# Optimization experiments

Measured on AMD Instinct MI355X. Metric: run time of the kernel, lower is better.

Reference implementation:

```python
import jax, jax.numpy as jnp
import numpy as np

N_LAYERS = 4
GAMMA = 0.5
D_MODEL = 256
D_STATE = 64
D_CONV = 4
EXPAND = 2
D_INNER = EXPAND * D_MODEL            # 512 (= headdim, so nheads = 1)
NHEADS = 1
CONV_DIM = D_INNER + 2 * D_STATE      # 640
D_IN_PROJ = 2 * D_INNER + 2 * D_STATE + NHEADS  # 1153
VOCAB = 100
VOCAB_PAD = 104                        # padded to multiple of 8 by MambaConfig
BATCH = 8
SEQ = 2048


def setup_inputs() -> dict:
    key = jax.random.key(0)
    ks = jax.random.split(key, 8)
    def nrm(k, shape):
        # gamma init: std = 1 / d1**gamma, d1 = shape[0]
        return (jax.random.normal(k, shape, jnp.float32) * (1.0 / shape[0] ** GAMMA))
    inp = {}
    inp["input_ids"] = jax.random.randint(ks[0], (BATCH, SEQ), 0, VOCAB)
    inp["embed"] = nrm(ks[1], (VOCAB_PAD, D_MODEL))          # tied embedding / lm_head
    inp["in_proj_w"] = nrm(ks[2], (N_LAYERS * D_IN_PROJ, D_MODEL)).reshape(N_LAYERS, D_IN_PROJ, D_MODEL)
    inp["conv_w"] = nrm(ks[3], (N_LAYERS * CONV_DIM, D_CONV)).reshape(N_LAYERS, CONV_DIM, D_CONV)
    inp["conv_b"] = jnp.zeros((N_LAYERS, CONV_DIM), jnp.float32)
    inp["dt_bias"] = jax.random.uniform(ks[4], (N_LAYERS, NHEADS), jnp.float32, -4.0, -1.0)
    inp["A_log"] = jnp.log(jax.random.uniform(ks[5], (N_LAYERS, NHEADS), jnp.float32, 1.0, 16.0))
    inp["Dparam"] = jnp.ones((N_LAYERS, NHEADS), jnp.float32)
    inp["norm_g_w"] = jnp.ones((N_LAYERS, D_INNER), jnp.float32)
    inp["out_proj_w"] = nrm(ks[6], (N_LAYERS * D_MODEL, D_INNER)).reshape(N_LAYERS, D_MODEL, D_INNER)
    inp["block_norm_w"] = jnp.ones((N_LAYERS, D_MODEL), jnp.float32)
    inp["norm_f_w"] = jnp.ones((D_MODEL,), jnp.float32)
    return inp


def rmsnorm(x, w, eps=1e-5):
    return x * jax.lax.rsqrt(jnp.mean(x * x, axis=-1, keepdims=True) + eps) * w


def ssm_scan(x, dt, A, Bc, Cc):
    # x: (B,L,P)  dt: (B,L)  A: scalar  Bc,Cc: (B,L,N). Sequential selective scan.
    def step(h, inp):  # h: (B,P,N)
        x_t, dt_t, b_t, c_t = inp
        h = h * jnp.exp(dt_t * A)[:, None, None] + (dt_t[:, None] * x_t)[:, :, None] * b_t[:, None, :]
        y = jnp.einsum('bpn,bn->bp', h, c_t)
        return h, y
    h0 = jnp.zeros((x.shape[0], x.shape[2], Bc.shape[2]), x.dtype)
    xs = (jnp.swapaxes(x, 0, 1), jnp.swapaxes(dt, 0, 1), jnp.swapaxes(Bc, 0, 1), jnp.swapaxes(Cc, 0, 1))
    _, ys = jax.lax.scan(step, h0, xs)
    return jnp.swapaxes(ys, 0, 1)  # (B,L,P)


def mamba2_mixer(h, ipw, cw, cb, dtb, alog, dp, ngw, opw):
    zxbcdt = h @ ipw.T                                   # (B,L,1153)
    z = zxbcdt[..., :D_INNER]
    xBC = zxbcdt[..., D_INNER:D_INNER + CONV_DIM]
    dt_raw = zxbcdt[..., D_INNER + CONV_DIM:]            # (B,L,1)
    # depthwise causal conv1d (kernel D_CONV) + SiLU
    xp = jnp.pad(xBC, ((0, 0), (D_CONV - 1, 0), (0, 0)))
    L = xBC.shape[1]
    conv = sum(xp[:, k:k + L, :] * cw[:, k] for k in range(D_CONV)) + cb
    xBC = jax.nn.silu(conv)
    x = xBC[..., :D_INNER]
    Bc = xBC[..., D_INNER:D_INNER + D_STATE]
    Cc = xBC[..., D_INNER + D_STATE:]
    dt = jax.nn.softplus(dt_raw[..., 0] + dtb[0])        # (B,L), nheads=1
    A = -jnp.exp(alog[0])
    y = ssm_scan(x, dt, A, Bc, Cc) + dp[0] * x
    y = rmsnorm(y * jax.nn.silu(z), ngw)                 # RMSNormGated (norm after gate)
    return y @ opw.T


def reference(input_ids, embed, in_proj_w, conv_w, conv_b, dt_bias, A_log, Dparam,
              norm_g_w, out_proj_w, block_norm_w, norm_f_w):
    hidden = embed[input_ids]                            # (B,L,D_MODEL)
    residual = None
    for i in range(N_LAYERS):
        residual = hidden if residual is None else hidden + residual
        hidden = rmsnorm(residual, block_norm_w[i])
        hidden = mamba2_mixer(hidden, in_proj_w[i], conv_w[i], conv_b[i], dt_bias[i],
                              A_log[i], Dparam[i], norm_g_w[i], out_proj_w[i])
    residual = hidden + residual
    final = rmsnorm(residual, norm_f_w)
    logits = final @ embed.T                             # tied lm_head, (B,L,VOCAB_PAD)
    return logits[:, -1, :VOCAB]                         # last-token logits, (B,VOCAB)
```

## Files before the change

kernel.cpp:

```cpp
#include <hip/hip_runtime.h>
#include <math.h>

#define NB    8
#define LSEQ  2048
#define TKN   16384
#define DM    256
#define DI    512
#define DS    64
#define DIP   1153
#define DIPP  1160
#define CDIM  640
#define NL    4
#define NC    16
#define CL    128
#define VOC   100

typedef short bf16x8 __attribute__((ext_vector_type(8)));
typedef short bf16x4 __attribute__((ext_vector_type(4)));
typedef float f32x4  __attribute__((ext_vector_type(4)));
typedef unsigned short ushort_t;

__device__ __forceinline__ unsigned short f2bf(float f) {
  unsigned int u = __float_as_uint(f);
  unsigned int r = u + 0x7FFFu + ((u >> 16) & 1u);
  return (unsigned short)(r >> 16);
}
__device__ __forceinline__ float bf2f(unsigned short u) {
  return __uint_as_float(((unsigned int)u) << 16);
}

__global__ __launch_bounds__(256) void prologue(const float* __restrict__ ipw,
    const float* __restrict__ opw, ushort_t* __restrict__ wbi, ushort_t* __restrict__ wbo,
    const int* __restrict__ ids, const float* __restrict__ embed,
    float* __restrict__ resid, ushort_t* __restrict__ hn, const float* __restrict__ w0) {
  int blk = blockIdx.x;
  if (blk < TKN / 4) {
    int wave = threadIdx.x >> 6, lane = threadIdx.x & 63;
    int t = blk * 4 + wave;
    size_t o = (size_t)t * DM + lane * 4;
    int id = ids[t];
    float4 r4 = *(const float4*)&embed[(size_t)id * DM + lane * 4];
    *(float4*)&resid[o] = r4;
    float ss = r4.x * r4.x + r4.y * r4.y + r4.z * r4.z + r4.w * r4.w;
    #pragma unroll
    for (int m = 32; m >= 1; m >>= 1) ss += __shfl_xor(ss, m, 64);
    float sc = rsqrtf(ss * (1.f / DM) + 1e-5f);
    float4 w4 = *(const float4*)&w0[lane * 4];
    bf16x4 o4;
    o4[0] = (short)f2bf(r4.x * sc * w4.x);
    o4[1] = (short)f2bf(r4.y * sc * w4.y);
    o4[2] = (short)f2bf(r4.z * sc * w4.z);
    o4[3] = (short)f2bf(r4.w * sc * w4.w);
    *(bf16x4*)&hn[o] = o4;
  } else {
    const int n1 = NL * DIP * DM;
    const int n2 = NL * DM * DI;
    int i4 = ((blk - TKN / 4) * 256 + threadIdx.x) * 4;
    if (i4 < n1) {
      float4 v = *(const float4*)(ipw + i4);
      bf16x4 o; o[0] = (short)f2bf(v.x); o[1] = (short)f2bf(v.y);
      o[2] = (short)f2bf(v.z); o[3] = (short)f2bf(v.w);
      *(bf16x4*)(wbi + i4) = o;
    } else {
      int j = i4 - n1;
      if (j < n2) {
        float4 v = *(const float4*)(opw + j);
        bf16x4 o; o[0] = (short)f2bf(v.x); o[1] = (short)f2bf(v.y);
        o[2] = (short)f2bf(v.z); o[3] = (short)f2bf(v.w);
        *(bf16x4*)(wbo + j) = o;
      }
    }
  }
}

#define LSTR  40
#define LSTR2 72
__global__ __launch_bounds__(256) void gemm_nt_bf16(const ushort_t* __restrict__ A,
    const ushort_t* __restrict__ Bw, ushort_t* __restrict__ C, int N, int K, int ldc) {
  __shared__ short sA[128 * LSTR2];
  __shared__ short sB[128 * LSTR2];
  int tid = threadIdx.x;
  int bn = blockIdx.x * 128;
  int bm = blockIdx.y * 128;
  int wave = tid >> 6, lane = tid & 63;
  int wm = (wave >> 1) * 64, wn = (wave & 1) * 64;
  int q = lane >> 4, c = lane & 15;

  f32x4 acc[4][4];
  #pragma unroll
  for (int i = 0; i < 4; ++i)
    #pragma unroll
    for (int j = 0; j < 4; ++j) acc[i][j] = (f32x4)0.f;

  int sr = tid >> 1;
  int sc = (tid & 1) * 32;
  const ushort_t* Ag = A + (size_t)(bm + sr) * K + sc;
  const ushort_t* Bg = Bw + (size_t)(bn + sr) * K + sc;
  bool bok = (bn + sr) < N;
  short* sAp = &sA[sr * LSTR2 + sc];
  short* sBp = &sB[sr * LSTR2 + sc];

  for (int k0 = 0; k0 < K; k0 += 64) {
    bf16x8 a0 = *(const bf16x8*)(Ag + k0);
    bf16x8 a1 = *(const bf16x8*)(Ag + k0 + 8);
    bf16x8 a2 = *(const bf16x8*)(Ag + k0 + 16);
    bf16x8 a3 = *(const bf16x8*)(Ag + k0 + 24);
    bf16x8 b0 = (bf16x8)(short)0, b1 = (bf16x8)(short)0;
    bf16x8 b2 = (bf16x8)(short)0, b3 = (bf16x8)(short)0;
    if (bok) {
      b0 = *(const bf16x8*)(Bg + k0);
      b1 = *(const bf16x8*)(Bg + k0 + 8);
      b2 = *(const bf16x8*)(Bg + k0 + 16);
      b3 = *(const bf16x8*)(Bg + k0 + 24);
    }
    __syncthreads();
    *(bf16x8*)(sAp)      = a0;
    *(bf16x8*)(sAp + 8)  = a1;
    *(bf16x8*)(sAp + 16) = a2;
    *(bf16x8*)(sAp + 24) = a3;
    *(bf16x8*)(sBp)      = b0;
    *(bf16x8*)(sBp + 8)  = b1;
    *(bf16x8*)(sBp + 16) = b2;
    *(bf16x8*)(sBp + 24) = b3;
    __syncthreads();
    #pragma unroll
    for (int ks = 0; ks < 2; ++ks) {
      bf16x8 af[4], bfr[4];
      #pragma unroll
      for (int i = 0; i < 4; ++i)
        af[i] = *(const bf16x8*)&sA[(wm + i * 16 + c) * LSTR2 + ks * 32 + q * 8];
      #pragma unroll
      for (int j = 0; j < 4; ++j)
        bfr[j] = *(const bf16x8*)&sB[(wn + j * 16 + c) * LSTR2 + ks * 32 + q * 8];
      #pragma unroll
      for (int i = 0; i < 4; ++i)
        #pragma unroll
        for (int j = 0; j < 4; ++j)
          acc[i][j] = __builtin_amdgcn_mfma_f32_16x16x32_bf16(af[i], bfr[j], acc[i][j], 0, 0, 0);
    }
  }
  #pragma unroll
  for (int i = 0; i < 4; ++i) {
    int m = bm + wm + i * 16 + q * 4;
    #pragma unroll
    for (int j = 0; j < 4; ++j) {
      int n = bn + wn + j * 16 + c;
      if (n < N) {
        #pragma unroll
        for (int r = 0; r < 4; ++r)
          C[(size_t)(m + r) * ldc + n] = f2bf(acc[i][j][r]);
      }
    }
  }
}

__global__ __launch_bounds__(256) void outproj_norm(const ushort_t* __restrict__ yb,
    const ushort_t* __restrict__ zx, const ushort_t* __restrict__ Bw,
    const float* __restrict__ gw, float* __restrict__ resid,
    const float* __restrict__ wnext, ushort_t* __restrict__ hn) {
  __shared__ short sA[32 * LSTR];
  __shared__ short sB[256 * LSTR];
  __shared__ float swl[DI];
  __shared__ float swn[DM];
  __shared__ float rs[128];
  __shared__ float rs2[32 * 2];
  int tid = threadIdx.x;
  int bm = blockIdx.x * 32;
  int wave = tid >> 6, lane = tid & 63;
  int wm = (wave >> 1) * 16, wn = (wave & 1) * 128;
  int q = lane >> 4, c = lane & 15;
  swl[tid] = gw[tid];
  swl[tid + 256] = gw[tid + 256];
  swn[tid] = wnext[tid];

  f32x4 acc[8];
  #pragma unroll
  for (int j = 0; j < 8; ++j) acc[j] = (f32x4)0.f;

  int ar = tid >> 2, ak = (tid & 3) * 8;
  bool isa = tid < 128;
  const ushort_t* yrow = yb + (size_t)(bm + ar) * DI + ak;
  const ushort_t* zrow = zx + (size_t)(bm + ar) * DIPP + ak;
  const ushort_t* Bg = Bw + (size_t)tid * DI;
  float sumsq = 0.f;
  __syncthreads();

  for (int k0 = 0; k0 < DI; k0 += 32) {
    bf16x8 g8;
    if (isa) {
      bf16x8 y8 = *(const bf16x8*)(yrow + k0);
      bf16x8 z8 = *(const bf16x8*)(zrow + k0);
      #pragma unroll
      for (int e = 0; e < 8; ++e) {
        float zz = bf2f((ushort_t)z8[e]);
        float gg = bf2f((ushort_t)y8[e]) * (zz / (1.f + __expf(-zz)));
        sumsq += gg * gg;
        g8[e] = (short)f2bf(gg * swl[k0 + ak + e]);
      }
    }
    bf16x8 b0 = *(const bf16x8*)(Bg + k0);
    bf16x8 b1 = *(const bf16x8*)(Bg + k0 + 8);
    bf16x8 b2 = *(const bf16x8*)(Bg + k0 + 16);
    bf16x8 b3 = *(const bf16x8*)(Bg + k0 + 24);
    __syncthreads();
    if (isa) *(bf16x8*)&sA[ar * LSTR + ak] = g8;
    *(bf16x8*)&sB[tid * LSTR]      = b0;
    *(bf16x8*)&sB[tid * LSTR + 8]  = b1;
    *(bf16x8*)&sB[tid * LSTR + 16] = b2;
    *(bf16x8*)&sB[tid * LSTR + 24] = b3;
    __syncthreads();
    bf16x8 af = *(const bf16x8*)&sA[(wm + c) * LSTR + q * 8];
    #pragma unroll
    for (int j = 0; j < 8; ++j) {
      bf16x8 bfr = *(const bf16x8*)&sB[(wn + j * 16 + c) * LSTR + q * 8];
      acc[j] = __builtin_amdgcn_mfma_f32_16x16x32_bf16(af, bfr, acc[j], 0, 0, 0);
    }
  }
  if (isa) rs[tid] = sumsq;
  __syncthreads();

  float outv[8][4];
  float sq2[4];
  #pragma unroll
  for (int r = 0; r < 4; ++r) {
    int row = wm + q * 4 + r;
    float s1 = rsqrtf((rs[row * 4] + rs[row * 4 + 1] + rs[row * 4 + 2] + rs[row * 4 + 3])
                      * (1.f / DI) + 1e-5f);
    float sq = 0.f;
    #pragma unroll
    for (int j = 0; j < 8; ++j) {
      int col = wn + j * 16 + c;
      size_t ro = (size_t)(bm + row) * DM + col;
      float rn = resid[ro] + s1 * acc[j][r];
      resid[ro] = rn;
      outv[j][r] = rn;
      sq += rn * rn;
    }
    sq2[r] = sq;
  }
  #pragma unroll
  for (int r = 0; r < 4; ++r) {
    #pragma unroll
    for (int m = 1; m <= 8; m <<= 1) sq2[r] += __shfl_xor(sq2[r], m, 64);
  }
  if (c == 0) {
    #pragma unroll
    for (int r = 0; r < 4; ++r)
      rs2[(wm + q * 4 + r) * 2 + (wave & 1)] = sq2[r];
  }
  __syncthreads();
  #pragma unroll
  for (int r = 0; r < 4; ++r) {
    int row = wm + q * 4 + r;
    float s2 = rsqrtf((rs2[row * 2] + rs2[row * 2 + 1]) * (1.f / DM) + 1e-5f);
    #pragma unroll
    for (int j = 0; j < 8; ++j) {
      int col = wn + j * 16 + c;
      hn[(size_t)(bm + row) * DM + col] = f2bf(outv[j][r] * s2 * swn[col]);
    }
  }
}

__global__ __launch_bounds__(256) void conv_silu(const ushort_t* __restrict__ zx,
    const float* __restrict__ cw, const float* __restrict__ cb,
    const float* __restrict__ dtbias, ushort_t* __restrict__ xo,
    ushort_t* __restrict__ Bo, ushort_t* __restrict__ Co, ushort_t* __restrict__ Ut,
    float* __restrict__ dtb, float* __restrict__ csumb) {
  __shared__ ushort_t tile[67 * 128];
  __shared__ ushort_t tt[128 * 72];
  int tid = threadIdx.x;
  int ct = blockIdx.x, tb_ = blockIdx.y, b = blockIdx.z;
  size_t rowb = (size_t)b * LSEQ;
  if (ct == 5) {
    if (tb_ < 16 && tid < 64) {
      int lane = tid;
      size_t base = rowb + (size_t)tb_ * CL;
      float bias = dtbias[0];
      float x0 = bf2f(zx[(base + 2 * lane) * DIPP + (DIP - 1)]) + bias;
      float x1 = bf2f(zx[(base + 2 * lane + 1) * DIPP + (DIP - 1)]) + bias;
      float d0 = (x0 > 20.f) ? x0 : log1pf(__expf(x0));
      float d1 = (x1 > 20.f) ? x1 : log1pf(__expf(x1));
      dtb[base + 2 * lane] = d0;
      dtb[base + 2 * lane + 1] = d1;
      float p = d0 + d1;
      #pragma unroll
      for (int off = 1; off < 64; off <<= 1) {
        float t = __shfl_up(p, off, 64);
        if (lane >= off) p += t;
      }
      csumb[base + 2 * lane]     = p - d1;
      csumb[base + 2 * lane + 1] = p;
    }
    return;
  }
  int c0 = ct * 128, l0 = tb_ * 64;
  bool isx = (ct < 4);
  for (int slot = tid; slot < 67 * 16; slot += 256) {
    int r = slot >> 4, gg = slot & 15;
    int l = l0 + r - 3;
    bf16x8 v = (bf16x8)(short)0;
    if (l >= 0) v = *(const bf16x8*)&zx[(rowb + l) * DIPP + DI + c0 + gg * 8];
    *(bf16x8*)&tile[r * 128 + gg * 8] = v;
  }
  int g = tid & 15, tq = tid >> 4;
  int cbase = c0 + g * 8;
  float w[4][8], bias[8];
  #pragma unroll
  for (int e = 0; e < 8; ++e) {
    float4 wv = *(const float4*)&cw[(cbase + e) * 4];
    w[0][e] = wv.x; w[1][e] = wv.y; w[2][e] = wv.z; w[3][e] = wv.w;
    bias[e] = cb[cbase + e];
  }
  __syncthreads();
  bf16x8 rows[7];
  #pragma unroll
  for (int r = 0; r < 7; ++r)
    rows[r] = *(const bf16x8*)&tile[(tq * 4 + r) * 128 + g * 8];
  #pragma unroll
  for (int it = 0; it < 4; ++it) {
    int t = tq * 4 + it;
    size_t tl = rowb + l0 + t;
    bf16x8 o;
    #pragma unroll
    for (int e = 0; e < 8; ++e) {
      float s = bias[e]
              + w[0][e] * bf2f((ushort_t)rows[it][e])
              + w[1][e] * bf2f((ushort_t)rows[it + 1][e])
              + w[2][e] * bf2f((ushort_t)rows[it + 2][e])
              + w[3][e] * bf2f((ushort_t)rows[it + 3][e]);
      float v = s / (1.f + __expf(-s));
      o[e] = (short)f2bf(v);
      if (isx) tt[(g * 8 + e) * 72 + t] = (ushort_t)o[e];
    }
    if (isx) {
      *(bf16x8*)&xo[tl * DI + cbase] = o;
    } else if (g < 8) {
      *(bf16x8*)&Bo[tl * DS + (cbase - DI)] = o;
    } else {
      *(bf16x8*)&Co[tl * DS + (cbase - DI - DS)] = o;
    }
  }
  if (isx) {
    __syncthreads();
    #pragma unroll
    for (int pass = 0; pass < 4; ++pass) {
      int slot = pass * 256 + tid;
      int op = slot >> 3, sg = slot & 7;
      bf16x8 v = *(const bf16x8*)&tt[op * 72 + sg * 8];
      *(bf16x8*)&Ut[((size_t)b * DI + c0 + op) * LSEQ + l0 + sg * 8] = v;
    }
  }
}

__global__ __launch_bounds__(256) void state_gemm(const ushort_t* __restrict__ Bb,
    const ushort_t* __restrict__ Ut, const float* __restrict__ csumb,
    const float* __restrict__ dtb, const float* __restrict__ alog,
    float* __restrict__ hst) {
  __shared__ short sW[64 * 144];
  __shared__ short sX[128 * 40];
  __shared__ float scs[128];
  __shared__ float sdt[128];
  int tid = threadIdx.x;
  int ph = blockIdx.x, ch = blockIdx.y, b = blockIdx.z;
  int bc = b * NC + ch;
  size_t tb = (size_t)b * LSEQ + ch * CL;
  float Aval = -expf(alog[0]);
  if (tid < 128) { scs[tid] = csumb[tb + tid]; sdt[tid] = dtb[tb + tid]; }
  __syncthreads();
  float Stot = scs[127];
  {
    int s = tid >> 1, noff = (tid & 1) * 32;
    float scale = __expf(Aval * (Stot - scs[s])) * sdt[s];
    #pragma unroll
    for (int blk = 0; blk < 4; ++blk) {
      bf16x8 v = *(const bf16x8*)&Bb[(tb + s) * DS + noff + blk * 8];
      #pragma unroll
      for (int e = 0; e < 8; ++e)
        sW[(noff + blk * 8 + e) * 144 + s] = (short)f2bf(bf2f((ushort_t)v[e]) * scale);
    }
  }
  int wave = tid >> 6, lane = tid & 63;
  int wn = (wave >> 1) * 32, wp = (wave & 1) * 64;
  int q = lane >> 4, c = lane & 15;
  f32x4 acc[2][4];
  #pragma unroll
  for (int i = 0; i < 2; ++i)
    #pragma unroll
    for (int j = 0; j < 4; ++j) acc[i][j] = (f32x4)0.f;

  for (int ks = 0; ks < 4; ++ks) {
    __syncthreads();
    {
      int r = tid >> 1, off = (tid & 1) * 16;
      size_t ua = ((size_t)b * DI + ph * 128 + r) * LSEQ + ch * CL + ks * 32 + off;
      bf16x8 u0 = *(const bf16x8*)&Ut[ua];
      bf16x8 u1 = *(const bf16x8*)&Ut[ua + 8];
      *(bf16x8*)&sX[r * 40 + off]     = u0;
      *(bf16x8*)&sX[r * 40 + off + 8] = u1;
    }
    __syncthreads();
    bf16x8 af[2], bfr[4];
    #pragma unroll
    for (int i = 0; i < 2; ++i)
      af[i] = *(const bf16x8*)&sW[(wn + i * 16 + c) * 144 + ks * 32 + q * 8];
    #pragma unroll
    for (int j = 0; j < 4; ++j)
      bfr[j] = *(const bf16x8*)&sX[(wp + j * 16 + c) * 40 + q * 8];
    #pragma unroll
    for (int i = 0; i < 2; ++i)
      #pragma unroll
      for (int j = 0; j < 4; ++j)
        acc[i][j] = __builtin_amdgcn_mfma_f32_16x16x32_bf16(af[i], bfr[j], acc[i][j], 0, 0, 0);
  }
  #pragma unroll
  for (int i = 0; i < 2; ++i) {
    int n = wn + i * 16 + q * 4;
    #pragma unroll
    for (int j = 0; j < 4; ++j) {
      int pg = ph * 128 + wp + j * 16 + c;
      #pragma unroll
      for (int r = 0; r < 4; ++r)
        hst[((size_t)bc * DS + n + r) * DI + pg] = acc[i][j][r];
    }
  }
}

__global__ __launch_bounds__(256) void combine2(const float* __restrict__ hst,
    const float* __restrict__ csumb, const float* __restrict__ alog,
    ushort_t* __restrict__ hin) {
  __shared__ ushort_t ts[64 * 17];
  int tid = threadIdx.x;
  int pt = blockIdx.x, nt = blockIdx.y, b = blockIdx.z;
  int p0 = pt * 64, n0 = nt * 16;
  int pl = tid & 63, ng = tid >> 6;
  float Aval = -expf(alog[0]);
  float h[4];
  #pragma unroll
  for (int i = 0; i < 4; ++i) h[i] = 0.f;
  for (int c = 0; c < NC; ++c) {
    int bc = b * NC + c;
    #pragma unroll
    for (int i = 0; i < 4; ++i)
      ts[pl * 17 + ng * 4 + i] = f2bf(h[i]);
    __syncthreads();
    {
      int on = tid & 15;
      #pragma unroll
      for (int pass = 0; pass < 4; ++pass) {
        int op = (tid >> 4) + pass * 16;
        hin[((size_t)bc * DI + p0 + op) * DS + n0 + on] = ts[op * 17 + on];
      }
    }
    __syncthreads();
    float Sc = csumb[(size_t)b * LSEQ + c * CL + CL - 1];
    float dec = __expf(Aval * Sc);
    #pragma unroll
    for (int i = 0; i < 4; ++i) {
      float loc = hst[((size_t)bc * DS + n0 + ng * 4 + i) * DI + p0 + pl];
      h[i] = h[i] * dec + loc;
    }
  }
}

__global__ __launch_bounds__(256) void y_gemm(const ushort_t* __restrict__ Bb,
    const ushort_t* __restrict__ Cb, const ushort_t* __restrict__ Ut,
    const ushort_t* __restrict__ hin, const float* __restrict__ csumb,
    const float* __restrict__ dtb, const float* __restrict__ alog,
    const float* __restrict__ dpar, const ushort_t* __restrict__ xb,
    ushort_t* __restrict__ y) {
  __shared__ short sC[128 * 72];
  __shared__ short sM[128 * 136];
  __shared__ short sU[128 * 80];
  __shared__ float scs[128];
  __shared__ float sdt[128];
  int tid = threadIdx.x;
  int ph = blockIdx.x, ch = blockIdx.y, b = blockIdx.z;
  int bc = b * NC + ch;
  size_t tb = (size_t)b * LSEQ + ch * CL;
  float Aval = -expf(alog[0]);
  float dp = dpar[0];
  int wave = tid >> 6, lane = tid & 63;
  int q = lane >> 4, c = lane & 15;

  {
    int r = tid >> 1, off = (tid & 1) * 32;
    #pragma unroll
    for (int blk = 0; blk < 4; ++blk) {
      *(bf16x8*)&sC[r * 72 + off + blk * 8] = *(const bf16x8*)&Cb[(tb + r) * DS + off + blk * 8];
      *(bf16x8*)&sU[r * 80 + off + blk * 8] = *(const bf16x8*)&Bb[(tb + r) * DS + off + blk * 8];
    }
  }
  if (tid < 128) { scs[tid] = csumb[tb + tid]; sdt[tid] = dtb[tb + tid]; }
  __syncthreads();

  {
    int wm = (wave >> 1) * 64, wss = (wave & 1) * 64;
    if (wave == 1) {
      #pragma unroll
      for (int i = 0; i < 4; ++i) {
        #pragma unroll
        for (int r = 0; r < 4; ++r) {
          int t = i * 16 + q * 4 + r;
          #pragma unroll
          for (int j = 0; j < 4; ++j)
            sM[t * 136 + 64 + j * 16 + c] = 0;
        }
      }
    } else {
      f32x4 g[4][4];
      #pragma unroll
      for (int i = 0; i < 4; ++i)
        #pragma unroll
        for (int j = 0; j < 4; ++j) g[i][j] = (f32x4)0.f;
      #pragma unroll
      for (int k0 = 0; k0 < 64; k0 += 32) {
        bf16x8 af[4], bfr[4];
        #pragma unroll
        for (int i = 0; i < 4; ++i)
          af[i] = *(const bf16x8*)&sC[(wm + i * 16 + c) * 72 + k0 + q * 8];
        #pragma unroll
        for (int j = 0; j < 4; ++j)
          bfr[j] = *(const bf16x8*)&sU[(wss + j * 16 + c) * 80 + k0 + q * 8];
        #pragma unroll
        for (int i = 0; i < 4; ++i)
          #pragma unroll
          for (int j = 0; j < 4; ++j)
            g[i][j] = __builtin_amdgcn_mfma_f32_16x16x32_bf16(af[i], bfr[j], g[i][j], 0, 0, 0);
      }
      float dts[4];
      #pragma unroll
      for (int j = 0; j < 4; ++j) dts[j] = sdt[wss + j * 16 + c];
      #pragma unroll
      for (int i = 0; i < 4; ++i) {
        #pragma unroll
        for (int r = 0; r < 4; ++r) {
          int t = wm + i * 16 + q * 4 + r;
          float ct = scs[t];
          #pragma unroll
          for (int j = 0; j < 4; ++j) {
            int s = wss + j * 16 + c;
            float v = g[i][j][r];
            float m = (s <= t) ? v * __expf(Aval * (ct - scs[s])) * dts[j] : 0.f;
            sM[t * 136 + s] = (short)f2bf(m);
          }
        }
      }
    }
  }

  int wm2 = (wave >> 1) * 64, wp = (wave & 1) * 64;
  f32x4 acc[4][4];
  #pragma unroll
  for (int i = 0; i < 4; ++i)
    #pragma unroll
    for (int j = 0; j < 4; ++j) acc[i][j] = (f32x4)0.f;

  for (int ks = 0; ks < 4; ++ks) {
    __syncthreads();
    {
      int r = tid >> 1, off = (tid & 1) * 16;
      size_t ua = ((size_t)b * DI + ph * 128 + r) * LSEQ + ch * CL + ks * 32 + off;
      bf16x8 u0 = *(const bf16x8*)&Ut[ua];
      bf16x8 u1 = *(const bf16x8*)&Ut[ua + 8];
      *(bf16x8*)&sU[r * 40 + off]     = u0;
      *(bf16x8*)&sU[r * 40 + off + 8] = u1;
    }
    __syncthreads();
    if (!(wm2 == 0 && ks >= 2)) {
      bf16x8 af[4], bfr[4];
      #pragma unroll
      for (int i = 0; i < 4; ++i)
        af[i] = *(const bf16x8*)&sM[(wm2 + i * 16 + c) * 136 + ks * 32 + q * 8];
      #pragma unroll
      for (int j = 0; j < 4; ++j)
        bfr[j] = *(const bf16x8*)&sU[(wp + j * 16 + c) * 40 + q * 8];
      #pragma unroll
      for (int i = 0; i < 4; ++i)
        #pragma unroll
        for (int j = 0; j < 4; ++j)
          acc[i][j] = __builtin_amdgcn_mfma_f32_16x16x32_bf16(af[i], bfr[j], acc[i][j], 0, 0, 0);
    }
  }

  __syncthreads();
  {
    int r = tid >> 1, off = (tid & 1) * 32;
    float sc_t = __expf(Aval * scs[r]);
    #pragma unroll
    for (int blk = 0; blk < 4; ++blk) {
      bf16x8 v = *(const bf16x8*)&sC[r * 72 + off + blk * 8];
      bf16x8 o;
      #pragma unroll
      for (int e = 0; e < 8; ++e)
        o[e] = (short)f2bf(bf2f((ushort_t)v[e]) * sc_t);
      *(bf16x8*)&sM[r * 80 + off + blk * 8] = o;
    }
  }
  for (int ks = 4; ks < 6; ++ks) {
    __syncthreads();
    {
      int r = tid >> 1, off = (tid & 1) * 16;
      size_t ha = ((size_t)bc * DI + ph * 128 + r) * DS + (ks - 4) * 32 + off;
      bf16x8 h0 = *(const bf16x8*)&hin[ha];
      bf16x8 h1 = *(const bf16x8*)&hin[ha + 8];
      *(bf16x8*)&sU[r * 40 + off]     = h0;
      *(bf16x8*)&sU[r * 40 + off + 8] = h1;
    }
    __syncthreads();
    bf16x8 af[4], bfr[4];
    #pragma unroll
    for (int i = 0; i < 4; ++i)
      af[i] = *(const bf16x8*)&sM[(wm2 + i * 16 + c) * 80 + (ks - 4) * 32 + q * 8];
    #pragma unroll
    for (int j = 0; j < 4; ++j)
      bfr[j] = *(const bf16x8*)&sU[(wp + j * 16 + c) * 40 + q * 8];
    #pragma unroll
    for (int i = 0; i < 4; ++i)
      #pragma unroll
      for (int j = 0; j < 4; ++j)
        acc[i][j] = __builtin_amdgcn_mfma_f32_16x16x32_bf16(af[i], bfr[j], acc[i][j], 0, 0, 0);
  }

  #pragma unroll
  for (int i = 0; i < 4; ++i) {
    #pragma unroll
    for (int r = 0; r < 4; ++r) {
      int t = wm2 + i * 16 + q * 4 + r;
      size_t row = (tb + t) * DI;
      #pragma unroll
      for (int j = 0; j < 4; ++j) {
        int pg = ph * 128 + wp + j * 16 + c;
        y[row + pg] = f2bf(acc[i][j][r] + dp * bf2f(xb[row + pg]));
      }
    }
  }
}

__global__ __launch_bounds__(256) void finalize(const ushort_t* __restrict__ hn,
    const float* __restrict__ embed, float* __restrict__ out) {
  int b = blockIdx.x, tid = threadIdx.x;
  __shared__ float fin[DM];
  size_t off = ((size_t)b * LSEQ + (LSEQ - 1)) * DM;
  fin[tid] = bf2f(hn[off + tid]);
  __syncthreads();
  if (tid < VOC) {
    float acc = 0.f;
    #pragma unroll 8
    for (int d = 0; d < DM; ++d) acc += fin[d] * embed[(size_t)tid * DM + d];
    out[b * VOC + tid] = acc;
  }
}

extern "C" void kernel_launch(void* const* d_in, const int* in_sizes, int n_in,
                              void* d_out, int out_size, void* d_ws, size_t ws_size,
                              hipStream_t stream) {
  const int*   ids   = (const int*)d_in[0];
  const float* embed = (const float*)d_in[1];
  const float* ipw   = (const float*)d_in[2];
  const float* cw    = (const float*)d_in[3];
  const float* cb    = (const float*)d_in[4];
  const float* dtbias= (const float*)d_in[5];
  const float* alog  = (const float*)d_in[6];
  const float* dpar  = (const float*)d_in[7];
  const float* ngw   = (const float*)d_in[8];
  const float* opw   = (const float*)d_in[9];
  const float* bnw   = (const float*)d_in[10];
  const float* nfw   = (const float*)d_in[11];
  float* out = (float*)d_out;

  char* p = (char*)d_ws;
  float* resid = (float*)p;            p += (size_t)TKN * DM * 4;
  ushort_t* hn = (ushort_t*)p;         p += (size_t)TKN * DM * 2;
  ushort_t* zx = (ushort_t*)p;         p += (size_t)TKN * DIPP * 2;
  float* dtb   = (float*)p;            p += (size_t)TKN * 4;
  float* csumb = (float*)p;            p += (size_t)TKN * 4;
  ushort_t* xb = (ushort_t*)p;         p += (size_t)TKN * DI * 2;
  ushort_t* yb = (ushort_t*)p;         p += (size_t)TKN * DI * 2;
  ushort_t* Bb = (ushort_t*)p;         p += (size_t)TKN * DS * 2;
  ushort_t* Cb = (ushort_t*)p;         p += (size_t)TKN * DS * 2;
  ushort_t* Ut = (ushort_t*)p;         p += (size_t)TKN * DI * 2;
  ushort_t* hin= (ushort_t*)p;         p += (size_t)NB * NC * DI * DS * 2;
  ushort_t* wbi= (ushort_t*)p;         p += (size_t)NL * DIP * DM * 2;
  ushort_t* wbo= (ushort_t*)p;         p += (size_t)NL * DM * DI * 2;
  float* hst = (float*)yb;

  const int convblks = (NL * DIP * DM + NL * DM * DI + 1023) / 1024;
  prologue<<<TKN / 4 + convblks, 256, 0, stream>>>(ipw, opw, wbi, wbo,
                                                   ids, embed, resid, hn, bnw);

  for (int i = 0; i < NL; ++i) {
    gemm_nt_bf16<<<dim3((DIP + 127) / 128, TKN / 128), 256, 0, stream>>>(
        hn, wbi + (size_t)i * DIP * DM, zx, DIP, DM, DIPP);
    conv_silu<<<dim3(6, LSEQ / 64, NB), 256, 0, stream>>>(
        zx, cw + (size_t)i * CDIM * 4, cb + (size_t)i * CDIM, dtbias + i,
        xb, Bb, Cb, Ut, dtb, csumb);
    state_gemm<<<dim3(4, NC, NB), 256, 0, stream>>>(Bb, Ut, csumb, dtb, alog + i, hst);
    combine2<<<dim3(DI / 64, 4, NB), 256, 0, stream>>>(hst, csumb, alog + i, hin);
    y_gemm<<<dim3(4, NC, NB), 256, 0, stream>>>(Bb, Cb, Ut, hin, csumb, dtb,
                                                alog + i, dpar + i, xb, yb);
    const float* wnext = (i < NL - 1) ? (bnw + (size_t)(i + 1) * DM) : nfw;
    outproj_norm<<<TKN / 32, 256, 0, stream>>>(
        yb, zx, wbo + (size_t)i * DM * DI, ngw + (size_t)i * DI, resid, wnext, hn);
  }

  finalize<<<NB, 256, 0, stream>>>(hn, embed, out);
}
```

Baseline: 544.0 us.

## Precompute masked C·Bᵀ decay matrix once per chunk in state_gemm, reuse in y_gemm

The intra-chunk masked decay matrix M (C·Bᵀ with exp decay and dt scaling) used to be rebuilt by every one of the 4 head-slice blocks in y_gemm. It is now computed once per (batch, chunk) by an extra block slice (ph==4) in state_gemm and written to a global bf16 buffer, which y_gemm then loads. y_gemm also scales C fragments in registers straight from global memory instead of staging them through shared memory, which cuts its LDS footprint. The cost is an extra global round trip of M (about 4MB per layer) and one more dependent block slice in state_gemm. The ph==4 blocks return early, with wave 1 doing no work and never writing the upper-right zero block. That block is never read, because y_gemm skips ks>=2 for rows 0-63.

```diff
diff --git a/kernel.cpp b/kernel.cpp
--- a/kernel.cpp
+++ b/kernel.cpp
@@ -353,11 +353,11 @@
 }
 
 __global__ __launch_bounds__(256) void state_gemm(const ushort_t* __restrict__ Bb,
-    const ushort_t* __restrict__ Ut, const float* __restrict__ csumb,
-    const float* __restrict__ dtb, const float* __restrict__ alog,
-    float* __restrict__ hst) {
-  __shared__ short sW[64 * 144];
-  __shared__ short sX[128 * 40];
+    const ushort_t* __restrict__ Cb, const ushort_t* __restrict__ Ut,
+    const float* __restrict__ csumb, const float* __restrict__ dtb,
+    const float* __restrict__ alog, float* __restrict__ hst,
+    ushort_t* __restrict__ Mbuf) {
+  __shared__ short smem[128 * 72 + 128 * 80];
   __shared__ float scs[128];
   __shared__ float sdt[128];
   int tid = threadIdx.x;
@@ -365,7 +365,71 @@
   int bc = b * NC + ch;
   size_t tb = (size_t)b * LSEQ + ch * CL;
   float Aval = -expf(alog[0]);
+  int wave = tid >> 6, lane = tid & 63;
+  int q = lane >> 4, c = lane & 15;
   if (tid < 128) { scs[tid] = csumb[tb + tid]; sdt[tid] = dtb[tb + tid]; }
+
+  if (ph == 4) {
+    short* sC = smem;
+    short* sB = smem + 128 * 72;
+    {
+      int r = tid >> 1, off = (tid & 1) * 32;
+      #pragma unroll
+      for (int blk = 0; blk < 4; ++blk) {
+        *(bf16x8*)&sC[r * 72 + off + blk * 8] = *(const bf16x8*)&Cb[(tb + r) * DS + off + blk * 8];
+        *(bf16x8*)&sB[r * 80 + off + blk * 8] = *(const bf16x8*)&Bb[(tb + r) * DS + off + blk * 8];
+      }
+    }
+    __syncthreads();
+    int wm = (wave >> 1) * 64, wss = (wave & 1) * 64;
+    if (wave == 1) return;
+    f32x4 g[4][4];
+    #pragma unroll
+    for (int i = 0; i < 4; ++i)
+      #pragma unroll
+      for (int j = 0; j < 4; ++j) g[i][j] = (f32x4)0.f;
+    #pragma unroll
+    for (int k0 = 0; k0 < 64; k0 += 32) {
+      bf16x8 af[4], bfr[4];
+      #pragma unroll
+      for (int i = 0; i < 4; ++i)
+        af[i] = *(const bf16x8*)&sC[(wm + i * 16 + c) * 72 + k0 + q * 8];
+      #pragma unroll
+      for (int j = 0; j < 4; ++j)
+        bfr[j] = *(const bf16x8*)&sB[(wss + j * 16 + c) * 80 + k0 + q * 8];
+      #pragma unroll
+      for (int i = 0; i < 4; ++i)
+        #pragma unroll
+        for (int j = 0; j < 4; ++j)
+          g[i][j] = __builtin_amdgcn_mfma_f32_16x16x32_bf16(af[i], bfr[j], g[i][j], 0, 0, 0);
+    }
+    float dts[4];
+    #pragma unroll
+    for (int j = 0; j < 4; ++j) dts[j] = sdt[wss + j * 16 + c];
+    ushort_t* Mrow = Mbuf + (size_t)bc * CL * CL;
+    #pragma unroll
+    for (int i = 0; i < 4; ++i) {
+      #pragma unroll
+      for (int r = 0; r < 4; ++r) {
+        int t = wm + i * 16 + q * 4 + r;
+        float ct = scs[t];
+        #pragma unroll
+        for (int j = 0; j < 4; ++j) {
+          int s = wss + j * 16 + c;
+          float v = g[i][j][r];
+          float m = (s <= t) ? v * __expf(Aval * (ct - scs[s])) * dts[j] : 0.f;
+          unsigned int mb = (unsigned int)f2bf(m);
+          unsigned int partner = __shfl_xor(mb, 1, 64);
+          if ((c & 1) == 0)
+            *(unsigned int*)&Mrow[t * CL + s] = mb | (partner << 16);
+        }
+      }
+    }
+    return;
+  }
+
+  short* sW = smem;
+  short* sX = smem + 64 * 144;
   __syncthreads();
   float Stot = scs[127];
   {
@@ -379,9 +443,7 @@
         sW[(noff + blk * 8 + e) * 144 + s] = (short)f2bf(bf2f((ushort_t)v[e]) * scale);
     }
   }
-  int wave = tid >> 6, lane = tid & 63;
   int wn = (wave >> 1) * 32, wp = (wave & 1) * 64;
-  int q = lane >> 4, c = lane & 15;
   f32x4 acc[2][4];
   #pragma unroll
   for (int i = 0; i < 2; ++i)
@@ -462,17 +524,14 @@
   }
 }
 
-__global__ __launch_bounds__(256) void y_gemm(const ushort_t* __restrict__ Bb,
+__global__ __launch_bounds__(256) void y_gemm(const ushort_t* __restrict__ Mbuf,
     const ushort_t* __restrict__ Cb, const ushort_t* __restrict__ Ut,
     const ushort_t* __restrict__ hin, const float* __restrict__ csumb,
-    const float* __restrict__ dtb, const float* __restrict__ alog,
-    const float* __restrict__ dpar, const ushort_t* __restrict__ xb,
-    ushort_t* __restrict__ y) {
-  __shared__ short sC[128 * 72];
+    const float* __restrict__ alog, const float* __restrict__ dpar,
+    const ushort_t* __restrict__ xb, ushort_t* __restrict__ y) {
   __shared__ short sM[128 * 136];
-  __shared__ short sU[128 * 80];
+  __shared__ short sU[128 * 40];
   __shared__ float scs[128];
-  __shared__ float sdt[128];
   int tid = threadIdx.x;
   int ph = blockIdx.x, ch = blockIdx.y, b = blockIdx.z;
   int bc = b * NC + ch;
@@ -483,72 +542,19 @@
   int q = lane >> 4, c = lane & 15;
 
   {
-    int r = tid >> 1, off = (tid & 1) * 32;
-    #pragma unroll
-    for (int blk = 0; blk < 4; ++blk) {
-      *(bf16x8*)&sC[r * 72 + off + blk * 8] = *(const bf16x8*)&Cb[(tb + r) * DS + off + blk * 8];
-      *(bf16x8*)&sU[r * 80 + off + blk * 8] = *(const bf16x8*)&Bb[(tb + r) * DS + off + blk * 8];
-    }
-  }
-  if (tid < 128) { scs[tid] = csumb[tb + tid]; sdt[tid] = dtb[tb + tid]; }
-  __syncthreads();
-
-  {
-    int wm = (wave >> 1) * 64, wss = (wave & 1) * 64;
-    if (wave == 1) {
-      #pragma unroll
-      for (int i = 0; i < 4; ++i) {
-        #pragma unroll
-        for (int r = 0; r < 4; ++r) {
-          int t = i * 16 + q * 4 + r;
-          #pragma unroll
-          for (int j = 0; j < 4; ++j)
-            sM[t * 136 + 64 + j * 16 + c] = 0;
-        }
-      }
-    } else {
-      f32x4 g[4][4];
-      #pragma unroll
-      for (int i = 0; i < 4; ++i)
-        #pragma unroll
-        for (int j = 0; j < 4; ++j) g[i][j] = (f32x4)0.f;
-      #pragma unroll
-      for (int k0 = 0; k0 < 64; k0 += 32) {
-        bf16x8 af[4], bfr[4];
-        #pragma unroll
-        for (int i = 0; i < 4; ++i)
-          af[i] = *(const bf16x8*)&sC[(wm + i * 16 + c) * 72 + k0 + q * 8];
-        #pragma unroll
-        for (int j = 0; j < 4; ++j)
-          bfr[j] = *(const bf16x8*)&sU[(wss + j * 16 + c) * 80 + k0 + q * 8];
-        #pragma unroll
-        for (int i = 0; i < 4; ++i)
-          #pragma unroll
-          for (int j = 0; j < 4; ++j)
-            g[i][j] = __builtin_amdgcn_mfma_f32_16x16x32_bf16(af[i], bfr[j], g[i][j], 0, 0, 0);
-      }
-      float dts[4];
-      #pragma unroll
-      for (int j = 0; j < 4; ++j) dts[j] = sdt[wss + j * 16 + c];
-      #pragma unroll
-      for (int i = 0; i < 4; ++i) {
-        #pragma unroll
-        for (int r = 0; r < 4; ++r) {
-          int t = wm + i * 16 + q * 4 + r;
-          float ct = scs[t];
-          #pragma unroll
-          for (int j = 0; j < 4; ++j) {
-            int s = wss + j * 16 + c;
-            float v = g[i][j][r];
-            float m = (s <= t) ? v * __expf(Aval * (ct - scs[s])) * dts[j] : 0.f;
-            sM[t * 136 + s] = (short)f2bf(m);
-          }
-        }
-      }
-    }
-  }
+    const ushort_t* Mrow = Mbuf + (size_t)bc * CL * CL;
+    #pragma unroll
+    for (int pass = 0; pass < 8; ++pass) {
+      int slot = pass * 256 + tid;
+      int t = slot >> 4, sg = slot & 15;
+      bf16x8 v = *(const bf16x8*)&Mrow[t * CL + sg * 8];
+      *(bf16x8*)&sM[t * 136 + sg * 8] = v;
+    }
+  }
+  if (tid < 128) scs[tid] = csumb[tb + tid];
 
   int wm2 = (wave >> 1) * 64, wp = (wave & 1) * 64;
+  int r2 = tid >> 1, off16 = (tid & 1) * 16;
   f32x4 acc[4][4];
   #pragma unroll
   for (int i = 0; i < 4; ++i)
@@ -558,12 +564,11 @@
   for (int ks = 0; ks < 4; ++ks) {
     __syncthreads();
     {
-      int r = tid >> 1, off = (tid & 1) * 16;
-      size_t ua = ((size_t)b * DI + ph * 128 + r) * LSEQ + ch * CL + ks * 32 + off;
+      size_t ua = ((size_t)b * DI + ph * 128 + r2) * LSEQ + ch * CL + ks * 32 + off16;
       bf16x8 u0 = *(const bf16x8*)&Ut[ua];
       bf16x8 u1 = *(const bf16x8*)&Ut[ua + 8];
-      *(bf16x8*)&sU[r * 40 + off]     = u0;
-      *(bf16x8*)&sU[r * 40 + off + 8] = u1;
+      *(bf16x8*)&sU[r2 * 40 + off16]     = u0;
+      *(bf16x8*)&sU[r2 * 40 + off16 + 8] = u1;
     }
     __syncthreads();
     if (!(wm2 == 0 && ks >= 2)) {
@@ -582,38 +587,31 @@
     }
   }
 
-  __syncthreads();
-  {
-    int r = tid >> 1, off = (tid & 1) * 32;
-    float sc_t = __expf(Aval * scs[r]);
-    #pragma unroll
-    for (int blk = 0; blk < 4; ++blk) {
-      bf16x8 v = *(const bf16x8*)&sC[r * 72 + off + blk * 8];
-      bf16x8 o;
-      #pragma unroll
-      for (int e = 0; e < 8; ++e)
-        o[e] = (short)f2bf(bf2f((ushort_t)v[e]) * sc_t);
-      *(bf16x8*)&sM[r * 80 + off + blk * 8] = o;
-    }
-  }
-  for (int ks = 4; ks < 6; ++ks) {
+  float rscale[4];
+  #pragma unroll
+  for (int i = 0; i < 4; ++i)
+    rscale[i] = __expf(Aval * scs[wm2 + i * 16 + c]);
+  for (int ks2 = 0; ks2 < 2; ++ks2) {
     __syncthreads();
     {
-      int r = tid >> 1, off = (tid & 1) * 16;
-      size_t ha = ((size_t)bc * DI + ph * 128 + r) * DS + (ks - 4) * 32 + off;
+      size_t ha = ((size_t)bc * DI + ph * 128 + r2) * DS + ks2 * 32 + off16;
       bf16x8 h0 = *(const bf16x8*)&hin[ha];
       bf16x8 h1 = *(const bf16x8*)&hin[ha + 8];
-      *(bf16x8*)&sU[r * 40 + off]     = h0;
-      *(bf16x8*)&sU[r * 40 + off + 8] = h1;
+      *(bf16x8*)&sU[r2 * 40 + off16]     = h0;
+      *(bf16x8*)&sU[r2 * 40 + off16 + 8] = h1;
     }
     __syncthreads();
     bf16x8 af[4], bfr[4];
-    #pragma unroll
-    for (int i = 0; i < 4; ++i)
-      af[i] = *(const bf16x8*)&sM[(wm2 + i * 16 + c) * 80 + (ks - 4) * 32 + q * 8];
     #pragma unroll
     for (int j = 0; j < 4; ++j)
       bfr[j] = *(const bf16x8*)&sU[(wp + j * 16 + c) * 40 + q * 8];
+    #pragma unroll
+    for (int i = 0; i < 4; ++i) {
+      bf16x8 cf = *(const bf16x8*)&Cb[(tb + wm2 + i * 16 + c) * DS + ks2 * 32 + q * 8];
+      #pragma unroll
+      for (int e = 0; e < 8; ++e)
+        af[i][e] = (short)f2bf(bf2f((ushort_t)cf[e]) * rscale[i]);
+    }
     #pragma unroll
     for (int i = 0; i < 4; ++i)
       #pragma unroll
@@ -682,6 +680,7 @@
   ushort_t* hin= (ushort_t*)p;         p += (size_t)NB * NC * DI * DS * 2;
   ushort_t* wbi= (ushort_t*)p;         p += (size_t)NL * DIP * DM * 2;
   ushort_t* wbo= (ushort_t*)p;         p += (size_t)NL * DM * DI * 2;
+  ushort_t* Mbuf=(ushort_t*)p;         p += (size_t)NB * NC * CL * CL * 2;
   float* hst = (float*)yb;
 
   const int convblks = (NL * DIP * DM + NL * DM * DI + 1023) / 1024;
@@ -694,9 +693,10 @@
     conv_silu<<<dim3(6, LSEQ / 64, NB), 256, 0, stream>>>(
         zx, cw + (size_t)i * CDIM * 4, cb + (size_t)i * CDIM, dtbias + i,
         xb, Bb, Cb, Ut, dtb, csumb);
-    state_gemm<<<dim3(4, NC, NB), 256, 0, stream>>>(Bb, Ut, csumb, dtb, alog + i, hst);
+    state_gemm<<<dim3(5, NC, NB), 256, 0, stream>>>(Bb, Cb, Ut, csumb, dtb,
+                                                    alog + i, hst, Mbuf);
     combine2<<<dim3(DI / 64, 4, NB), 256, 0, stream>>>(hst, csumb, alog + i, hin);
-    y_gemm<<<dim3(4, NC, NB), 256, 0, stream>>>(Bb, Cb, Ut, hin, csumb, dtb,
+    y_gemm<<<dim3(4, NC, NB), 256, 0, stream>>>(Mbuf, Cb, Ut, hin, csumb,
                                                 alog + i, dpar + i, xb, yb);
     const float* wnext = (i < NL - 1) ? (bnw + (size_t)(i + 1) * DM) : nfw;
     outproj_norm<<<TKN / 32, 256, 0, stream>>>(
```

Result: no change. 548.7 us (+0.9%).
